# Kernel tuning notes

Hardware: AMD Instinct MI355X
Metric: run time of the kernel (lower is better)

## Reference

```python
import jax, jax.numpy as jnp
import numpy as np

B, N, M, D = 8, 4096, 4096, 3

def setup_inputs() -> dict:
    key = jax.random.key(0)
    ks = jax.random.split(key, 6)
    return {
        "X_pred": jax.random.normal(ks[0], (B, N, D), dtype=jnp.float32),
        "X_true": jax.random.normal(ks[1], (B, M, D), dtype=jnp.float32),
        "R_pred": jax.random.normal(ks[2], (B, D, D), dtype=jnp.float32),
        "t_pred": jax.random.normal(ks[3], (B, D), dtype=jnp.float32),
        "R_true": jax.random.normal(ks[4], (B, D, D), dtype=jnp.float32),
        "t_true": jax.random.normal(ks[5], (B, D), dtype=jnp.float32),
        "temperature": jnp.asarray(0.1, dtype=jnp.float32),
    }

def reference(X_pred, X_true, R_pred, t_pred, R_true, t_true, temperature):
    # Rigid transforms: x' = R x + t
    Xp = jnp.einsum('bij,bnj->bni', R_pred, X_pred) + t_pred[:, None, :]  # (B,N,D)
    Xt = jnp.einsum('bij,bmj->bmi', R_true, X_true) + t_true[:, None, :]  # (B,M,D)
    # Squared pairwise distances: |a|^2 + |b|^2 - 2 a.b  (== cdist(p=2)**2)
    sq_p = jnp.sum(Xp * Xp, axis=-1)  # (B,N)
    sq_t = jnp.sum(Xt * Xt, axis=-1)  # (B,M)
    dist_sq = sq_p[:, :, None] + sq_t[:, None, :] - 2.0 * jnp.einsum('bnd,bmd->bnm', Xp, Xt)
    dist_sq = jnp.maximum(dist_sq, 0.0)  # (B,N,M)
    soft_alignment = jax.nn.softmax(-dist_sq / temperature, axis=-1)
    weighted_distances = jnp.sum(soft_alignment * dist_sq, axis=-1)  # (B,N)
    return jnp.mean(weighted_distances)
```

## Files before the change

### kernel.cpp

```cpp
#include <hip/hip_runtime.h>


#define B_    8
#define N_    4096
#define M_    4096
#define NWAVE 8
#define BLOCK (NWAVE * 64)
#define ROWS  512
#define MSPL  16
#define QCH   (M_ / MSPL)
#define WQ    (QCH / NWAVE)
#define LOG2E 1.4426950408889634f
#define LN2   0.6931471805599453f
#define BIGF  3.0e38f

typedef float v2f __attribute__((ext_vector_type(2)));

__global__ __launch_bounds__(BLOCK, 6) void softfape_main(
    const float* __restrict__ X_pred, const float* __restrict__ X_true,
    const float* __restrict__ R_pred, const float* __restrict__ t_pred,
    const float* __restrict__ R_true, const float* __restrict__ t_true,
    const float* __restrict__ temp,
    float4* __restrict__ Pg)
{
    __shared__ float4 Q[QCH];
    __shared__ float  Wp[NWAVE][ROWS];
    __shared__ float  shl[ROWS];
    __shared__ float  pwl[ROWS];

    const int tid  = threadIdx.x;
    const int wave = tid >> 6;
    const int lane = tid & 63;
    const int x    = blockIdx.x;
    const int ms   = x & 15;
    const int rg   = (x >> 4) & 7;
    const int b    = x >> 7;

    const float T   = temp[0];
    const float c   = LOG2E / T;
    const float m2c = -2.0f * c;

    if (tid < QCH / 2) {
        const float g00 = R_true[b*9+0], g01 = R_true[b*9+1], g02 = R_true[b*9+2];
        const float g10 = R_true[b*9+3], g11 = R_true[b*9+4], g12 = R_true[b*9+5];
        const float g20 = R_true[b*9+6], g21 = R_true[b*9+7], g22 = R_true[b*9+8];
        const float u0  = t_true[b*3+0], u1 = t_true[b*3+1], u2 = t_true[b*3+2];
        const float2* xt = (const float2*)(X_true + ((size_t)b * M_ + ms * QCH) * 3);
        const float2 f0 = xt[3*tid+0], f1 = xt[3*tid+1], f2 = xt[3*tid+2];
        {
            const float y0 = fmaf(g00, f0.x, fmaf(g01, f0.y, fmaf(g02, f1.x, u0)));
            const float y1 = fmaf(g10, f0.x, fmaf(g11, f0.y, fmaf(g12, f1.x, u1)));
            const float y2 = fmaf(g20, f0.x, fmaf(g21, f0.y, fmaf(g22, f1.x, u2)));
            const float nn = fmaf(y0, y0, fmaf(y1, y1, y2 * y2));
            Q[2*tid]   = make_float4(m2c*y0, m2c*y1, m2c*y2, c*nn);
        }
        {
            const float y0 = fmaf(g00, f1.y, fmaf(g01, f2.x, fmaf(g02, f2.y, u0)));
            const float y1 = fmaf(g10, f1.y, fmaf(g11, f2.x, fmaf(g12, f2.y, u1)));
            const float y2 = fmaf(g20, f1.y, fmaf(g21, f2.x, fmaf(g22, f2.y, u2)));
            const float nn = fmaf(y0, y0, fmaf(y1, y1, y2 * y2));
            Q[2*tid+1] = make_float4(m2c*y0, m2c*y1, m2c*y2, c*nn);
        }
    }

    v2f px2[4], py2[4], pz2[4];
    {
        const float h00 = R_pred[b*9+0], h01 = R_pred[b*9+1], h02 = R_pred[b*9+2];
        const float h10 = R_pred[b*9+3], h11 = R_pred[b*9+4], h12 = R_pred[b*9+5];
        const float h20 = R_pred[b*9+6], h21 = R_pred[b*9+7], h22 = R_pred[b*9+8];
        const float v0 = t_pred[b*3+0], v1 = t_pred[b*3+1], v2 = t_pred[b*3+2];
        const float4* xp = (const float4*)(X_pred + ((size_t)b * N_ + rg * ROWS + lane * 8) * 3);
        const float4 a0 = xp[0], a1 = xp[1], a2 = xp[2];
        const float4 a3 = xp[3], a4 = xp[4], a5 = xp[5];
        const float rx[8] = {a0.x, a0.w, a1.z, a2.y, a3.x, a3.w, a4.z, a5.y};
        const float ry[8] = {a0.y, a1.x, a1.w, a2.z, a3.y, a4.x, a4.w, a5.z};
        const float rz[8] = {a0.z, a1.y, a2.x, a2.w, a3.z, a4.y, a5.x, a5.w};
        #pragma unroll
        for (int j = 0; j < 8; ++j) {
            const float ppx = fmaf(h00, rx[j], fmaf(h01, ry[j], fmaf(h02, rz[j], v0)));
            const float ppy = fmaf(h10, rx[j], fmaf(h11, ry[j], fmaf(h12, rz[j], v1)));
            const float ppz = fmaf(h20, rx[j], fmaf(h21, ry[j], fmaf(h22, rz[j], v2)));
            px2[j >> 1][j & 1] = ppx;
            py2[j >> 1][j & 1] = ppy;
            pz2[j >> 1][j & 1] = ppz;
            if (wave == 0) pwl[8*lane + j] = c * fmaf(ppx, ppx, fmaf(ppy, ppy, ppz * ppz));
        }
    }

    __syncthreads();

    const float4* __restrict__ Qw = Q + wave * WQ;

    v2f mA2[4] = {{BIGF, BIGF}, {BIGF, BIGF}, {BIGF, BIGF}, {BIGF, BIGF}};
    #pragma unroll 4
    for (int k = 0; k < WQ; ++k) {
        const float4 q = Qw[k];
        const v2f qx = {q.x, q.x}, qy = {q.y, q.y}, qz = {q.z, q.z}, qw = {q.w, q.w};
        #pragma unroll
        for (int j = 0; j < 4; ++j) {
            const v2f A = qx * px2[j] + (qy * py2[j] + (qz * pz2[j] + qw));
            mA2[j] = __builtin_elementwise_min(mA2[j], A);
        }
    }
    #pragma unroll
    for (int j = 0; j < 4; ++j) {
        Wp[wave][8*lane + 2*j]     = mA2[j].x;
        Wp[wave][8*lane + 2*j + 1] = mA2[j].y;
    }
    __syncthreads();

    {
        float m = Wp[0][tid];
        #pragma unroll
        for (int w2 = 1; w2 < NWAVE; ++w2) m = fminf(m, Wp[w2][tid]);
        shl[tid] = m;
    }
    __syncthreads();

    v2f sh2[4];
    {
        const float4 s0 = *(const float4*)&shl[8*lane];
        const float4 s1 = *(const float4*)&shl[8*lane + 4];
        sh2[0] = (v2f){s0.x, s0.y};  sh2[1] = (v2f){s0.z, s0.w};
        sh2[2] = (v2f){s1.x, s1.y};  sh2[3] = (v2f){s1.z, s1.w};
    }

    v2f L2[4]  = {{0.f,0.f},{0.f,0.f},{0.f,0.f},{0.f,0.f}};
    v2f SA2[4] = {{0.f,0.f},{0.f,0.f},{0.f,0.f},{0.f,0.f}};
    #pragma unroll 4
    for (int k = 0; k < WQ; ++k) {
        const float4 q = Qw[k];
        const v2f qx = {q.x, q.x}, qy = {q.y, q.y}, qz = {q.z, q.z}, qw = {q.w, q.w};
        #pragma unroll
        for (int j = 0; j < 4; ++j) {
            const v2f A   = qx * px2[j] + (qy * py2[j] + (qz * pz2[j] + qw));
            const v2f arg = sh2[j] - A;
            const v2f w   = {__builtin_amdgcn_exp2f(arg.x),
                             __builtin_amdgcn_exp2f(arg.y)};
            L2[j]  += w;
            SA2[j]  = w * arg + SA2[j];
        }
    }

    #pragma unroll
    for (int j = 0; j < 4; ++j) {
        Wp[wave][8*lane + 2*j]     = L2[j].x;
        Wp[wave][8*lane + 2*j + 1] = L2[j].y;
    }
    __syncthreads();
    float Lr = 0.0f;
    #pragma unroll
    for (int w2 = 0; w2 < NWAVE; ++w2) Lr += Wp[w2][tid];
    __syncthreads();
    #pragma unroll
    for (int j = 0; j < 4; ++j) {
        Wp[wave][8*lane + 2*j]     = SA2[j].x;
        Wp[wave][8*lane + 2*j + 1] = SA2[j].y;
    }
    __syncthreads();
    float Sr = 0.0f;
    #pragma unroll
    for (int w2 = 0; w2 < NWAVE; ++w2) Sr += Wp[w2][tid];

    {
        const size_t row = (size_t)b * N_ + rg * ROWS + tid;
        Pg[(size_t)ms * (B_ * N_) + row] = make_float4(shl[tid] + pwl[tid], Lr, Sr, 0.0f);
    }
}

__global__ __launch_bounds__(256) void softfape_finalize(
    const float4* __restrict__ Pg, const float* __restrict__ temp,
    float* __restrict__ out)
{
    __shared__ float ws4[4];
    const int tid = threadIdx.x;
    const size_t row = (size_t)blockIdx.x * 256 + tid;

    float4 P[MSPL];
    #pragma unroll
    for (int i = 0; i < MSPL; ++i) P[i] = Pg[(size_t)i * (B_ * N_) + row];

    float m = P[0].x;
    #pragma unroll
    for (int i = 1; i < MSPL; ++i) m = fminf(m, P[i].x);

    float L = 0.0f, SA = 0.0f;
    #pragma unroll
    for (int i = 0; i < MSPL; ++i) {
        const float dm = m - P[i].x;
        const float f  = __builtin_amdgcn_exp2f(dm);
        L  = fmaf(P[i].y, f, L);
        SA = fmaf(f, fmaf(dm, P[i].y, P[i].z), SA);
    }
    float wd = m - SA / L;

    wd += __shfl_xor(wd, 1);  wd += __shfl_xor(wd, 2);  wd += __shfl_xor(wd, 4);
    wd += __shfl_xor(wd, 8);  wd += __shfl_xor(wd, 16); wd += __shfl_xor(wd, 32);
    if ((tid & 63) == 0) ws4[tid >> 6] = wd;
    __syncthreads();
    if (tid == 0) {
        const float s = ws4[0] + ws4[1] + ws4[2] + ws4[3];
        const float scale = temp[0] * LN2 / ((float)B_ * (float)N_);
        atomicAdd(out, s * scale);
    }
}

extern "C" void kernel_launch(void* const* d_in, const int* in_sizes, int n_in,
                              void* d_out, int out_size, void* d_ws, size_t ws_size,
                              hipStream_t stream) {
    const float* X_pred = (const float*)d_in[0];
    const float* X_true = (const float*)d_in[1];
    const float* R_pred = (const float*)d_in[2];
    const float* t_pred = (const float*)d_in[3];
    const float* R_true = (const float*)d_in[4];
    const float* t_true = (const float*)d_in[5];
    const float* temp   = (const float*)d_in[6];
    float* out = (float*)d_out;

    float4* Pg = (float4*)d_ws;

    hipMemsetAsync(out, 0, sizeof(float), stream);

    softfape_main<<<dim3(B_ * 8 * MSPL), BLOCK, 0, stream>>>(
        X_pred, X_true, R_pred, t_pred, R_true, t_true, temp, Pg);

    softfape_finalize<<<dim3((B_ * N_) / 256), 256, 0, stream>>>(Pg, temp, out);
}
```

Before: 105.6 us.

## Estimate per-wave row max in fp16 and rescale after the exp pass

The first min-pass over the query points now runs in packed fp16 FMAs, using a half-precision copy of Q kept in shared memory. Each wave then uses its own approximate shift in the exp pass, with no wait for a cross-wave reduction. The exact cross-wave min is computed afterwards and the per-wave L and SA accumulators are rescaled by exp2 of the difference. This removes two block barriers between the passes and halves the cost of the min pass. The risk is that fp16 rounding or overflow (values above about 65504, tied to the 0.1 temperature scaling) leaves a poor shift, which could overflow or underflow the exp terms and lose accuracy.

```diff
diff --git a/kernel.cpp b/kernel.cpp
--- a/kernel.cpp
+++ b/kernel.cpp
@@ -14,7 +14,8 @@
 #define LN2   0.6931471805599453f
 #define BIGF  3.0e38f
 
-typedef float v2f __attribute__((ext_vector_type(2)));
+typedef float    v2f __attribute__((ext_vector_type(2)));
+typedef _Float16 h2  __attribute__((ext_vector_type(2)));
 
 __global__ __launch_bounds__(BLOCK, 6) void softfape_main(
     const float* __restrict__ X_pred, const float* __restrict__ X_true,
@@ -23,6 +24,7 @@
     const float* __restrict__ temp,
     float4* __restrict__ Pg)
 {
+    __shared__ uint4  Qh[QCH];
     __shared__ float4 Q[QCH];
     __shared__ float  Wp[NWAVE][ROWS];
     __shared__ float  shl[ROWS];
@@ -47,23 +49,32 @@
         const float u0  = t_true[b*3+0], u1 = t_true[b*3+1], u2 = t_true[b*3+2];
         const float2* xt = (const float2*)(X_true + ((size_t)b * M_ + ms * QCH) * 3);
         const float2 f0 = xt[3*tid+0], f1 = xt[3*tid+1], f2 = xt[3*tid+2];
-        {
-            const float y0 = fmaf(g00, f0.x, fmaf(g01, f0.y, fmaf(g02, f1.x, u0)));
-            const float y1 = fmaf(g10, f0.x, fmaf(g11, f0.y, fmaf(g12, f1.x, u1)));
-            const float y2 = fmaf(g20, f0.x, fmaf(g21, f0.y, fmaf(g22, f1.x, u2)));
+        #pragma unroll
+        for (int e = 0; e < 2; ++e) {
+            const float xx = e ? f1.y : f0.x;
+            const float yy = e ? f2.x : f0.y;
+            const float zz = e ? f2.y : f1.x;
+            const float y0 = fmaf(g00, xx, fmaf(g01, yy, fmaf(g02, zz, u0)));
+            const float y1 = fmaf(g10, xx, fmaf(g11, yy, fmaf(g12, zz, u1)));
+            const float y2 = fmaf(g20, xx, fmaf(g21, yy, fmaf(g22, zz, u2)));
             const float nn = fmaf(y0, y0, fmaf(y1, y1, y2 * y2));
-            Q[2*tid]   = make_float4(m2c*y0, m2c*y1, m2c*y2, c*nn);
-        }
-        {
-            const float y0 = fmaf(g00, f1.y, fmaf(g01, f2.x, fmaf(g02, f2.y, u0)));
-            const float y1 = fmaf(g10, f1.y, fmaf(g11, f2.x, fmaf(g12, f2.y, u1)));
-            const float y2 = fmaf(g20, f1.y, fmaf(g21, f2.x, fmaf(g22, f2.y, u2)));
-            const float nn = fmaf(y0, y0, fmaf(y1, y1, y2 * y2));
-            Q[2*tid+1] = make_float4(m2c*y0, m2c*y1, m2c*y2, c*nn);
+            const float qx = m2c * y0, qy = m2c * y1, qz = m2c * y2, qw = c * nn;
+            Q[2*tid + e] = make_float4(qx, qy, qz, qw);
+            const h2 hx = {(_Float16)qx, (_Float16)qx};
+            const h2 hy = {(_Float16)qy, (_Float16)qy};
+            const h2 hz = {(_Float16)qz, (_Float16)qz};
+            const h2 hw = {(_Float16)qw, (_Float16)qw};
+            uint4 u;
+            u.x = __builtin_bit_cast(unsigned, hx);
+            u.y = __builtin_bit_cast(unsigned, hy);
+            u.z = __builtin_bit_cast(unsigned, hz);
+            u.w = __builtin_bit_cast(unsigned, hw);
+            Qh[2*tid + e] = u;
         }
     }
 
     v2f px2[4], py2[4], pz2[4];
+    h2  hpx[4], hpy[4], hpz[4];
     {
         const float h00 = R_pred[b*9+0], h01 = R_pred[b*9+1], h02 = R_pred[b*9+2];
         const float h10 = R_pred[b*9+3], h11 = R_pred[b*9+4], h12 = R_pred[b*9+5];
@@ -83,47 +94,39 @@
             px2[j >> 1][j & 1] = ppx;
             py2[j >> 1][j & 1] = ppy;
             pz2[j >> 1][j & 1] = ppz;
+            hpx[j >> 1][j & 1] = (_Float16)ppx;
+            hpy[j >> 1][j & 1] = (_Float16)ppy;
+            hpz[j >> 1][j & 1] = (_Float16)ppz;
             if (wave == 0) pwl[8*lane + j] = c * fmaf(ppx, ppx, fmaf(ppy, ppy, ppz * ppz));
         }
     }
 
     __syncthreads();
 
-    const float4* __restrict__ Qw = Q + wave * WQ;
-
-    v2f mA2[4] = {{BIGF, BIGF}, {BIGF, BIGF}, {BIGF, BIGF}, {BIGF, BIGF}};
+    const uint4*  __restrict__ Qhw = Qh + wave * WQ;
+    const float4* __restrict__ Qw  = Q  + wave * WQ;
+
+    h2 mH[4];
+    #pragma unroll
+    for (int j = 0; j < 4; ++j) mH[j] = (h2){(_Float16)30000.0f, (_Float16)30000.0f};
     #pragma unroll 4
     for (int k = 0; k < WQ; ++k) {
-        const float4 q = Qw[k];
-        const v2f qx = {q.x, q.x}, qy = {q.y, q.y}, qz = {q.z, q.z}, qw = {q.w, q.w};
+        const uint4 qq = Qhw[k];
+        const h2 hqx = __builtin_bit_cast(h2, qq.x);
+        const h2 hqy = __builtin_bit_cast(h2, qq.y);
+        const h2 hqz = __builtin_bit_cast(h2, qq.z);
+        const h2 hqw = __builtin_bit_cast(h2, qq.w);
         #pragma unroll
         for (int j = 0; j < 4; ++j) {
-            const v2f A = qx * px2[j] + (qy * py2[j] + (qz * pz2[j] + qw));
-            mA2[j] = __builtin_elementwise_min(mA2[j], A);
-        }
-    }
-    #pragma unroll
-    for (int j = 0; j < 4; ++j) {
-        Wp[wave][8*lane + 2*j]     = mA2[j].x;
-        Wp[wave][8*lane + 2*j + 1] = mA2[j].y;
-    }
-    __syncthreads();
-
-    {
-        float m = Wp[0][tid];
-        #pragma unroll
-        for (int w2 = 1; w2 < NWAVE; ++w2) m = fminf(m, Wp[w2][tid]);
-        shl[tid] = m;
-    }
-    __syncthreads();
-
+            const h2 Ah = __builtin_elementwise_fma(hqx, hpx[j],
+                          __builtin_elementwise_fma(hqy, hpy[j],
+                          __builtin_elementwise_fma(hqz, hpz[j], hqw)));
+            mH[j] = __builtin_elementwise_min(mH[j], Ah);
+        }
+    }
     v2f sh2[4];
-    {
-        const float4 s0 = *(const float4*)&shl[8*lane];
-        const float4 s1 = *(const float4*)&shl[8*lane + 4];
-        sh2[0] = (v2f){s0.x, s0.y};  sh2[1] = (v2f){s0.z, s0.w};
-        sh2[2] = (v2f){s1.x, s1.y};  sh2[3] = (v2f){s1.z, s1.w};
-    }
+    #pragma unroll
+    for (int j = 0; j < 4; ++j) sh2[j] = (v2f){(float)mH[j].x, (float)mH[j].y};
 
     v2f L2[4]  = {{0.f,0.f},{0.f,0.f},{0.f,0.f},{0.f,0.f}};
     v2f SA2[4] = {{0.f,0.f},{0.f,0.f},{0.f,0.f},{0.f,0.f}};
@@ -139,6 +142,33 @@
                              __builtin_amdgcn_exp2f(arg.y)};
             L2[j]  += w;
             SA2[j]  = w * arg + SA2[j];
+        }
+    }
+
+    #pragma unroll
+    for (int j = 0; j < 4; ++j) {
+        Wp[wave][8*lane + 2*j]     = sh2[j].x;
+        Wp[wave][8*lane + 2*j + 1] = sh2[j].y;
+    }
+    __syncthreads();
+    {
+        float m = Wp[0][tid];
+        #pragma unroll
+        for (int w2 = 1; w2 < NWAVE; ++w2) m = fminf(m, Wp[w2][tid]);
+        shl[tid] = m;
+    }
+    __syncthreads();
+
+    {
+        const float4 s0 = *(const float4*)&shl[8*lane];
+        const float4 s1 = *(const float4*)&shl[8*lane + 4];
+        const v2f g2[4] = {{s0.x, s0.y}, {s0.z, s0.w}, {s1.x, s1.y}, {s1.z, s1.w}};
+        #pragma unroll
+        for (int j = 0; j < 4; ++j) {
+            const v2f dl = g2[j] - sh2[j];
+            const v2f f  = {__builtin_amdgcn_exp2f(dl.x), __builtin_amdgcn_exp2f(dl.y)};
+            SA2[j] = f * (SA2[j] + dl * L2[j]);
+            L2[j]  = f * L2[j];
         }
     }
 
```

Measured after the change: 104.4 us. No clear change (-1.2%).
